# Kernel optimization log

Measured on AMD Instinct MI355X. Metric: run time of the kernel, lower is better.

The kernel has to match this reference:

```python
import jax, jax.numpy as jnp
import numpy as np

DIM = 512
WIN = 8
HEADS = 16
HEAD_DIM = DIM // HEADS
N = WIN * WIN
B_ = 1568


def _rel_pos_idx(window_size: int) -> np.ndarray:
    ch = np.arange(window_size)
    cw = np.arange(window_size)
    coords = np.stack(np.meshgrid(ch, cw, indexing='ij'))  # [2, W, W]
    flat = coords.reshape(2, -1)                            # [2, N]
    rel = flat[:, :, None] - flat[:, None, :]               # [2, N, N]
    rel = rel.transpose(1, 2, 0).copy()                     # [N, N, 2]
    rel[:, :, 0] += window_size - 1
    rel[:, :, 1] += window_size - 1
    rel[:, :, 0] *= 2 * window_size - 1
    return rel.sum(-1).astype(np.int32)                     # [N, N]


def setup_inputs() -> dict:
    key = jax.random.key(0)
    kx, kt, kq, kp, kb = jax.random.split(key, 5)
    x = jax.random.normal(kx, (B_, N, DIM), dtype=jnp.float32)
    # learned params
    table = jax.random.normal(kt, ((2 * WIN - 1) ** 2, HEADS), dtype=jnp.float32) * 0.02
    qkv_w = jax.random.normal(kq, (3 * DIM, DIM), dtype=jnp.float32) * (1.0 / np.sqrt(DIM))
    proj_w = jax.random.normal(kp, (DIM, DIM), dtype=jnp.float32) * (1.0 / np.sqrt(DIM))
    proj_b = jax.random.normal(kb, (DIM,), dtype=jnp.float32) * 0.02
    rel_idx = jnp.asarray(_rel_pos_idx(WIN))  # [N, N] int32
    return {"x": x, "qkv_w": qkv_w, "table": table, "proj_w": proj_w,
            "proj_b": proj_b, "rel_idx": rel_idx}


def reference(x, qkv_w, table, proj_w, proj_b, rel_idx):
    Bw, n, c = x.shape
    scale = jnp.sqrt(jnp.float32(HEAD_DIM))
    # qkv: Linear no-bias, torch weight [3C, C] -> x @ W^T
    qkv = (x @ qkv_w.T).reshape(Bw, n, 3, HEADS, HEAD_DIM)
    qkv = jnp.transpose(qkv, (2, 0, 3, 1, 4))  # [3, B, H, N, hd]
    q, k, v = qkv[0], qkv[1], qkv[2]
    attn = jnp.einsum('bhnd,bhmd->bhnm', q, k) / scale  # [B, H, N, N]
    bias = table[rel_idx]                                # [N, N, H]
    attn = attn + jnp.transpose(bias, (2, 0, 1))[None]   # [B, H, N, N]
    attn = jax.nn.softmax(attn, axis=-1)
    out = jnp.einsum('bhnm,bhmd->bhnd', attn, v)         # [B, H, N, hd]
    out = jnp.transpose(out, (0, 2, 1, 3)).reshape(Bw, n, c)
    return out @ proj_w.T + proj_b
```

## Files before the change

kernel.cpp:

```cpp
#include <hip/hip_runtime.h>
#include <stdint.h>

typedef unsigned short ushort_t;
typedef unsigned long long u64_t;
typedef __attribute__((ext_vector_type(4))) float f32x4;
typedef __attribute__((ext_vector_type(8))) short s16x8;

#define S1_ELEMS ((size_t)1568*64*512)

__device__ __forceinline__ ushort_t f2bf(float f) {
  unsigned u = __builtin_bit_cast(unsigned, f);
  u = u + 0x7fffu + ((u >> 16) & 1u);
  return (ushort_t)(u >> 16);
}

__device__ __forceinline__ void gl_lds16(const ushort_t* g, ushort_t* l) {
  typedef __attribute__((address_space(1))) void gvoid;
  typedef __attribute__((address_space(3))) void lvoid;
  __builtin_amdgcn_global_load_lds((gvoid*)(ushort_t*)g, (lvoid*)l, 16, 0, 0);
}

__global__ void k_prep(const float* __restrict__ x, ushort_t* __restrict__ xh,
                       const float* __restrict__ wq, ushort_t* __restrict__ wqh,
                       const float* __restrict__ wp, ushort_t* __restrict__ wph,
                       const float* __restrict__ table, const int* __restrict__ rel_idx,
                       float* __restrict__ bias) {
  int blk = blockIdx.x, tid = threadIdx.x;
  if (blk < 3136) {
    long i0 = (long)blk*256 + tid;
    #pragma unroll
    for (int rep = 0; rep < 8; rep++) {
      long i = i0 + (long)rep*802816;
      float4 v0 = ((const float4*)x)[2*i];
      float4 v1 = ((const float4*)x)[2*i + 1];
      s16x8 pk;
      pk[0] = (short)f2bf(v0.x); pk[1] = (short)f2bf(v0.y);
      pk[2] = (short)f2bf(v0.z); pk[3] = (short)f2bf(v0.w);
      pk[4] = (short)f2bf(v1.x); pk[5] = (short)f2bf(v1.y);
      pk[6] = (short)f2bf(v1.z); pk[7] = (short)f2bf(v1.w);
      *(s16x8*)&xh[i*8] = pk;
    }
  } else if (blk < 3648) {
    const float* src; ushort_t* dst; long i;
    if (blk < 3520) { src = wq; dst = wqh; i = (long)(blk - 3136)*256 + tid; }
    else            { src = wp; dst = wph; i = (long)(blk - 3520)*256 + tid; }
    float4 v0 = ((const float4*)src)[2*i];
    float4 v1 = ((const float4*)src)[2*i + 1];
    s16x8 pk;
    pk[0] = (short)f2bf(v0.x); pk[1] = (short)f2bf(v0.y);
    pk[2] = (short)f2bf(v0.z); pk[3] = (short)f2bf(v0.w);
    pk[4] = (short)f2bf(v1.x); pk[5] = (short)f2bf(v1.y);
    pk[6] = (short)f2bf(v1.z); pk[7] = (short)f2bf(v1.w);
    *(s16x8*)&dst[i*8] = pk;
  } else {
    int i0 = ((blk - 3648)*256 + tid)*4;
    #pragma unroll
    for (int j = 0; j < 4; j++) {
      int i = i0 + j;
      int h = i >> 12, rc = i & 4095;
      bias[i] = table[rel_idx[rc] * 16 + h];
    }
  }
}

struct GemmCtx {
  ushort_t* lds;
  const ushort_t *pA0, *pA1, *pB0, *pB1;
  int w, lane, wm, wn;
};

template<int BUFP, int KH, int RH, int SSEL, int SBUFP, int SU, int VM>
__device__ __forceinline__ void phase(const GemmCtx& C, f32x4 (&acc)[8][4], s16x8 (&bf)[4], int stau) {
  s16x8 af[4];
  #pragma unroll
  for (int t = 0; t < 4; t++)
    af[t] = *(const s16x8*)&C.lds[BUFP*32768 + ((C.wm*8 + RH*4 + t)*2 + KH)*512 + C.lane*8];
  if constexpr (RH == 0) {
    #pragma unroll
    for (int t = 0; t < 4; t++)
      bf[t] = *(const s16x8*)&C.lds[BUFP*32768 + 16384 + ((C.wn*4 + t)*2 + KH)*512 + C.lane*8];
  }
  if constexpr (SSEL == 0) {
    gl_lds16(C.pA0 + stau*64 + SU*32, C.lds + SBUFP*32768 + (4*C.w + SU)*512);
    gl_lds16(C.pA1 + stau*64 + SU*32, C.lds + SBUFP*32768 + (4*C.w + 2 + SU)*512);
  } else if constexpr (SSEL == 1) {
    gl_lds16(C.pB0 + stau*64 + SU*32, C.lds + SBUFP*32768 + 16384 + (4*C.w + SU)*512);
    gl_lds16(C.pB1 + stau*64 + SU*32, C.lds + SBUFP*32768 + 16384 + (4*C.w + 2 + SU)*512);
  }
  if constexpr (VM == 8) asm volatile("s_waitcnt vmcnt(8)" ::: "memory");
  else if constexpr (VM == 4) asm volatile("s_waitcnt vmcnt(4)" ::: "memory");
  else if constexpr (VM == 0) asm volatile("s_waitcnt vmcnt(0)" ::: "memory");
  __builtin_amdgcn_s_barrier();
  __builtin_amdgcn_s_setprio(1);
  #pragma unroll
  for (int ta = 0; ta < 4; ta++)
    #pragma unroll
    for (int tb = 0; tb < 4; tb++)
      acc[RH*4 + ta][tb] = __builtin_amdgcn_mfma_f32_16x16x32_bf16(af[ta], bf[tb], acc[RH*4 + ta][tb], 0, 0, 0);
  __builtin_amdgcn_s_setprio(0);
  __builtin_amdgcn_s_barrier();
}

template<int BUFP, bool S12, bool S34, int VM2, int VM4>
__device__ __forceinline__ void ktile(const GemmCtx& C, f32x4 (&acc)[8][4], int tau) {
  s16x8 bf[4];
  phase<BUFP, 0, 0, S12 ? 0 : -1, BUFP^1, 1, -1 >(C, acc, bf, tau + 1);
  phase<BUFP, 0, 1, S12 ? 1 : -1, BUFP^1, 1, VM2>(C, acc, bf, tau + 1);
  phase<BUFP, 1, 0, S34 ? 0 : -1, BUFP,   0, -1 >(C, acc, bf, tau + 2);
  phase<BUFP, 1, 1, S34 ? 1 : -1, BUFP,   0, VM4>(C, acc, bf, tau + 2);
}

__global__ __launch_bounds__(512, 2) void k_gemm_qkv(
    const ushort_t* __restrict__ xh, const ushort_t* __restrict__ wh,
    ushort_t* __restrict__ qh, ushort_t* __restrict__ kh, ushort_t* __restrict__ vt) {
  extern __shared__ __align__(16) ushort_t lds[];
  const int tid = threadIdx.x, w = tid >> 6, lane = tid & 63;
  const int g = lane >> 4, l15 = lane & 15;
  const int wm = w >> 2, wn = w & 3;
  int flat = blockIdx.x;
  int swz = (flat & 7) * 294 + (flat >> 3);
  int bx = swz % 6, by = swz / 6;

  GemmCtx C;
  C.lds = lds;
  C.pA0 = xh + ((size_t)by*256 + (size_t)(2*w)*16 + l15)*512 + g*8;
  C.pA1 = C.pA0 + 16*512;
  C.pB0 = wh + ((size_t)bx*256 + (size_t)(2*w)*16 + l15)*512 + g*8;
  C.pB1 = C.pB0 + 16*512;
  C.w = w; C.lane = lane; C.wm = wm; C.wn = wn;

  f32x4 acc[8][4];
  #pragma unroll
  for (int r = 0; r < 8; r++)
    #pragma unroll
    for (int c = 0; c < 4; c++) acc[r][c] = (f32x4){0.f, 0.f, 0.f, 0.f};

  gl_lds16(C.pA0 +  0, lds + (4*w + 0)*512);
  gl_lds16(C.pA1 +  0, lds + (4*w + 2)*512);
  gl_lds16(C.pB0 +  0, lds + 16384 + (4*w + 0)*512);
  gl_lds16(C.pB1 +  0, lds + 16384 + (4*w + 2)*512);
  gl_lds16(C.pA0 + 32, lds + (4*w + 1)*512);
  gl_lds16(C.pA1 + 32, lds + (4*w + 3)*512);
  gl_lds16(C.pB0 + 32, lds + 16384 + (4*w + 1)*512);
  gl_lds16(C.pB1 + 32, lds + 16384 + (4*w + 3)*512);
  gl_lds16(C.pA0 + 64, lds + 32768 + (4*w + 0)*512);
  gl_lds16(C.pA1 + 64, lds + 32768 + (4*w + 2)*512);
  gl_lds16(C.pB0 + 64, lds + 32768 + 16384 + (4*w + 0)*512);
  gl_lds16(C.pB1 + 64, lds + 32768 + 16384 + (4*w + 2)*512);
  asm volatile("s_waitcnt vmcnt(4)" ::: "memory");
  __builtin_amdgcn_s_barrier();

  for (int kt = 0; kt < 6; kt += 2) {
    ktile<0, true, true, 8, 8>(C, acc, kt);
    ktile<1, true, true, 8, 8>(C, acc, kt + 1);
  }
  ktile<0, true,  false, 8, 4>(C, acc, 6);
  ktile<1, false, false, 0, -1>(C, acc, 7);

  asm volatile("" ::: "memory");
  const int sel = bx >> 1;
  if (sel < 2) {
    #pragma unroll
    for (int ra = 0; ra < 8; ra++)
      #pragma unroll
      for (int tb = 0; tb < 4; tb++)
        #pragma unroll
        for (int j = 0; j < 4; j++) {
          int row = wm*128 + ra*16 + g*4 + j;
          int col = wn*64 + tb*16 + l15;
          int r = (row >> 6)*8 + (col >> 5);
          int n = row & 63, d = col & 31;
          int byte = r*4096 + ((n*64 + d*2) ^ ((n & 12) << 3));
          *(ushort_t*)((char*)lds + byte) = f2bf(acc[ra][tb][j]);
        }
  } else {
    #pragma unroll
    for (int ra = 0; ra < 8; ra++)
      #pragma unroll
      for (int tb = 0; tb < 4; tb++) {
        int row0 = wm*128 + ra*16 + g*4;
        int col = wn*64 + tb*16 + l15;
        int r = (row0 >> 6)*8 + (col >> 5);
        int n0 = row0 & 63, d = col & 31;
        u64_t pk = (u64_t)f2bf(acc[ra][tb][0])
                 | ((u64_t)f2bf(acc[ra][tb][1]) << 16)
                 | ((u64_t)f2bf(acc[ra][tb][2]) << 32)
                 | ((u64_t)f2bf(acc[ra][tb][3]) << 48);
        int byte = r*4096 + ((d*128 + n0*2) ^ ((d & 7) << 4) ^ (((((d >> 3) ^ (n0 >> 3))) & 1) << 6));
        *(u64_t*)((char*)lds + byte) = pk;
      }
  }
  asm volatile("s_waitcnt lgkmcnt(0)" ::: "memory");
  __builtin_amdgcn_s_barrier();
  ushort_t* dst = (sel == 0) ? qh : (sel == 1) ? kh : vt;
  const int hbase = (bx & 1) * 8;
  #pragma unroll
  for (int it = 0; it < 16; it++) {
    int cg = it*512 + tid;
    int r = cg >> 8, inner = cg & 255;
    int byte;
    if (sel < 2) byte = r*4096 + ((inner*16) ^ (((inner >> 2) & 12) << 3));
    else         byte = r*4096 + ((inner*16) ^ (((inner >> 3) & 7) << 4) ^ ((((inner >> 6) ^ inner) & 1) << 6));
    s16x8 v = *(const s16x8*)((const char*)lds + byte);
    int b = by*4 + (r >> 3), h = hbase + (r & 7);
    *(s16x8*)&dst[(size_t)(b*16 + h)*2048 + inner*8] = v;
  }
}

__device__ __forceinline__ void gemm256_loop(
    ushort_t* lds, const ushort_t* pA, const ushort_t* pB,
    int w, int lane, int wm, int wn, f32x4 (&acc)[8][4]) {
  #pragma unroll
  for (int q = 0; q < 2; q++) {
    gl_lds16(pA + q*8192 +  0, lds + ((2*w + q)*2 + 0)*512);
    gl_lds16(pA + q*8192 + 32, lds + ((2*w + q)*2 + 1)*512);
    gl_lds16(pB + q*8192 +  0, lds + 16384 + ((2*w + q)*2 + 0)*512);
    gl_lds16(pB + q*8192 + 32, lds + 16384 + ((2*w + q)*2 + 1)*512);
  }
  asm volatile("s_waitcnt vmcnt(0)" ::: "memory");
  __builtin_amdgcn_s_barrier();

  for (int tau = 0; tau < 8; ++tau) {
    ushort_t* bufR = lds + (tau & 1)*32768;
    ushort_t* bufW = lds + ((tau & 1) ^ 1)*32768;
    if (tau < 7) {
      int ko = (tau + 1)*64;
      #pragma unroll
      for (int q = 0; q < 2; q++) {
        gl_lds16(pA + q*8192 + ko,      bufW + ((2*w + q)*2 + 0)*512);
        gl_lds16(pA + q*8192 + ko + 32, bufW + ((2*w + q)*2 + 1)*512);
        gl_lds16(pB + q*8192 + ko,      bufW + 16384 + ((2*w + q)*2 + 0)*512);
        gl_lds16(pB + q*8192 + ko + 32, bufW + 16384 + ((2*w + q)*2 + 1)*512);
      }
    }
    s16x8 af[4][2], bf[4][2];
    #pragma unroll
    for (int t = 0; t < 4; t++)
      #pragma unroll
      for (int kh = 0; kh < 2; kh++) {
        af[t][kh] = *(const s16x8*)&bufR[((wm*8 + t)*2 + kh)*512 + lane*8];
        bf[t][kh] = *(const s16x8*)&bufR[16384 + ((wn*4 + t)*2 + kh)*512 + lane*8];
      }
    __builtin_amdgcn_s_barrier();
    asm volatile("s_waitcnt lgkmcnt(0)" ::: "memory");
    __builtin_amdgcn_sched_barrier(0);
    __builtin_amdgcn_s_setprio(1);
    #pragma unroll
    for (int t = 0; t < 4; t++)
      #pragma unroll
      for (int tb = 0; tb < 4; tb++) {
        acc[t][tb] = __builtin_amdgcn_mfma_f32_16x16x32_bf16(af[t][0], bf[tb][0], acc[t][tb], 0, 0, 0);
        acc[t][tb] = __builtin_amdgcn_mfma_f32_16x16x32_bf16(af[t][1], bf[tb][1], acc[t][tb], 0, 0, 0);
      }
    __builtin_amdgcn_s_setprio(0);
    s16x8 ag[4][2];
    #pragma unroll
    for (int t = 0; t < 4; t++)
      #pragma unroll
      for (int kh = 0; kh < 2; kh++)
        ag[t][kh] = *(const s16x8*)&bufR[((wm*8 + 4 + t)*2 + kh)*512 + lane*8];
    asm volatile("s_waitcnt lgkmcnt(0)" ::: "memory");
    __builtin_amdgcn_sched_barrier(0);
    __builtin_amdgcn_s_setprio(1);
    #pragma unroll
    for (int t = 0; t < 4; t++)
      #pragma unroll
      for (int tb = 0; tb < 4; tb++) {
        acc[4 + t][tb] = __builtin_amdgcn_mfma_f32_16x16x32_bf16(ag[t][0], bf[tb][0], acc[4 + t][tb], 0, 0, 0);
        acc[4 + t][tb] = __builtin_amdgcn_mfma_f32_16x16x32_bf16(ag[t][1], bf[tb][1], acc[4 + t][tb], 0, 0, 0);
      }
    __builtin_amdgcn_s_setprio(0);
    asm volatile("s_waitcnt vmcnt(0)" ::: "memory");
    __builtin_amdgcn_s_barrier();
  }
}

__global__ __launch_bounds__(512, 2) void k_gemm_proj(
    const ushort_t* __restrict__ ah, const ushort_t* __restrict__ wh,
    const float* __restrict__ pb, float* __restrict__ out) {
  extern __shared__ __align__(16) ushort_t lds[];
  const int tid = threadIdx.x, w = tid >> 6, lane = tid & 63;
  const int g = lane >> 4, l15 = lane & 15;
  const int wm = w >> 2, wn = w & 3;
  int flat = blockIdx.x;
  int swz = (flat & 7) * 98 + (flat >> 3);
  int bx = swz & 1, by = swz >> 1;

  const ushort_t* pA = ah + ((size_t)by*256 + (size_t)(2*w)*16 + l15)*512 + g*8;
  const ushort_t* pB = wh + ((size_t)bx*256 + (size_t)(2*w)*16 + l15)*512 + g*8;

  f32x4 acc[8][4];
  #pragma unroll
  for (int r = 0; r < 8; r++)
    #pragma unroll
    for (int c = 0; c < 4; c++) acc[r][c] = (f32x4){0.f, 0.f, 0.f, 0.f};

  gemm256_loop(lds, pA, pB, w, lane, wm, wn, acc);

  asm volatile("" ::: "memory");
  #pragma unroll
  for (int p = 0; p < 2; p++) {
    if (p) { asm volatile("" ::: "memory"); __builtin_amdgcn_s_barrier(); }
    if (wm == p) {
      #pragma unroll
      for (int ra = 0; ra < 8; ra++)
        #pragma unroll
        for (int tb = 0; tb < 4; tb++)
          #pragma unroll
          for (int j = 0; j < 4; j++) {
            int row = ra*16 + g*4 + j;
            int col = wn*64 + tb*16 + l15;
            int byte = (row*1024 + col*4) ^ ((row & 12) << 2) ^ ((row & 8) << 3);
            *(float*)((char*)lds + byte) = acc[ra][tb][j];
          }
    }
    asm volatile("s_waitcnt lgkmcnt(0)" ::: "memory");
    __builtin_amdgcn_s_barrier();
    #pragma unroll
    for (int it = 0; it < 16; it++) {
      int cg = it*512 + tid;
      int row = cg >> 6, c16 = cg & 63;
      int byte = row*1024 + ((c16*16) ^ ((row & 12) << 2) ^ ((row & 8) << 3));
      f32x4 v = *(const f32x4*)((const char*)lds + byte);
      int ncol = bx*256 + c16*4;
      f32x4 pbv = *(const f32x4*)&pb[ncol];
      v = v + pbv;
      *(f32x4*)&out[(size_t)(by*256 + p*128 + row)*512 + ncol] = v;
    }
  }
}

__global__ __launch_bounds__(256) void k_attn(
    const ushort_t* __restrict__ qh, const ushort_t* __restrict__ kh,
    const ushort_t* __restrict__ vt, const float* __restrict__ bias,
    ushort_t* __restrict__ aoh) {
  __shared__ ushort_t plds[4][4096];
  __shared__ float blds[64*68];
  const int tid = threadIdx.x, w = tid >> 6, lane = tid & 63;
  const int g = lane >> 4, l15 = lane & 15;
  const int h = blockIdx.x & 15;
  const int b = (blockIdx.x >> 4)*4 + w;
  const size_t base = (size_t)(b*16 + h) * 2048;

  s16x8 qf[4], kf[4];
  #pragma unroll
  for (int t = 0; t < 4; t++) {
    size_t o = base + (size_t)(t*16 + l15)*32 + g*8;
    qf[t] = *(const s16x8*)&qh[o];
    kf[t] = *(const s16x8*)&kh[o];
  }
  s16x8 vf[2][2];
  #pragma unroll
  for (int kt = 0; kt < 2; kt++)
    #pragma unroll
    for (int nt = 0; nt < 2; nt++)
      vf[kt][nt] = *(const s16x8*)&vt[base + (size_t)(nt*16 + l15)*64 + kt*32 + g*8];

  const float* bh_ = bias + ((size_t)h << 12);
  #pragma unroll
  for (int it = 0; it < 4; it++) {
    int idx = it*1024 + tid*4;
    int rr = idx >> 6, cc = idx & 63;
    *(f32x4*)&blds[rr*68 + cc] = *(const f32x4*)&bh_[idx];
  }
  __syncthreads();

  f32x4 s[4][4];
  #pragma unroll
  for (int r = 0; r < 4; r++)
    #pragma unroll
    for (int c = 0; c < 4; c++) s[r][c] = (f32x4){0.f,0.f,0.f,0.f};
  #pragma unroll
  for (int r = 0; r < 4; r++)
    #pragma unroll
    for (int c = 0; c < 4; c++)
      s[r][c] = __builtin_amdgcn_mfma_f32_16x16x32_bf16(qf[r], kf[c], s[r][c], 0, 0, 0);

  const float invs = 0.17677669529663687f;
  #pragma unroll
  for (int r = 0; r < 4; r++)
    #pragma unroll
    for (int c = 0; c < 4; c++)
      #pragma unroll
      for (int j = 0; j < 4; j++) {
        int rr = r*16 + g*4 + j, cc = c*16 + l15;
        s[r][c][j] = s[r][c][j]*invs + blds[rr*68 + cc];
      }

  #pragma unroll
  for (int r = 0; r < 4; r++)
    #pragma unroll
    for (int j = 0; j < 4; j++) {
      float mx = fmaxf(fmaxf(s[r][0][j], s[r][1][j]), fmaxf(s[r][2][j], s[r][3][j]));
      mx = fmaxf(mx, __shfl_xor(mx, 1));
      mx = fmaxf(mx, __shfl_xor(mx, 2));
      mx = fmaxf(mx, __shfl_xor(mx, 4));
      mx = fmaxf(mx, __shfl_xor(mx, 8));
      float p0 = __expf(s[r][0][j]-mx), p1 = __expf(s[r][1][j]-mx);
      float p2 = __expf(s[r][2][j]-mx), p3 = __expf(s[r][3][j]-mx);
      float sum = p0 + p1 + p2 + p3;
      sum += __shfl_xor(sum, 1);
      sum += __shfl_xor(sum, 2);
      sum += __shfl_xor(sum, 4);
      sum += __shfl_xor(sum, 8);
      float rv = 1.0f / sum;
      s[r][0][j] = p0*rv; s[r][1][j] = p1*rv; s[r][2][j] = p2*rv; s[r][3][j] = p3*rv;
    }

  ushort_t* Pw = plds[w];
  asm volatile("s_waitcnt lgkmcnt(0)" ::: "memory");
  __builtin_amdgcn_sched_barrier(0);
  #pragma unroll
  for (int r = 0; r < 4; r++)
    #pragma unroll
    for (int c = 0; c < 4; c++)
      #pragma unroll
      for (int j = 0; j < 4; j++) {
        int idx = ((c >> 1)*4 + r)*512 + ((((c & 1)*2) + (l15 >> 3))*16 + g*4 + j)*8 + (l15 & 7);
        Pw[idx] = f2bf(s[r][c][j]);
      }
  asm volatile("s_waitcnt lgkmcnt(0)" ::: "memory");
  __builtin_amdgcn_sched_barrier(0);

  s16x8 pf[4][2];
  #pragma unroll
  for (int ta = 0; ta < 4; ta++)
    #pragma unroll
    for (int kt = 0; kt < 2; kt++)
      pf[ta][kt] = *(const s16x8*)&Pw[(kt*4 + ta)*512 + lane*8];

  f32x4 o[4][2];
  #pragma unroll
  for (int ta = 0; ta < 4; ta++)
    #pragma unroll
    for (int nt = 0; nt < 2; nt++) o[ta][nt] = (f32x4){0.f,0.f,0.f,0.f};
  #pragma unroll
  for (int ta = 0; ta < 4; ta++)
    #pragma unroll
    for (int nt = 0; nt < 2; nt++)
      #pragma unroll
      for (int kt = 0; kt < 2; kt++)
        o[ta][nt] = __builtin_amdgcn_mfma_f32_16x16x32_bf16(pf[ta][kt], vf[kt][nt], o[ta][nt], 0, 0, 0);

  #pragma unroll
  for (int ta = 0; ta < 4; ta++)
    #pragma unroll
    for (int nt = 0; nt < 2; nt++)
      #pragma unroll
      for (int j = 0; j < 4; j++) {
        int rr = ta*16 + g*4 + j, dd = nt*16 + l15;
        aoh[((size_t)b*64 + rr)*512 + h*32 + dd] = f2bf(o[ta][nt][j]);
      }
}

extern "C" void kernel_launch(void* const* d_in, const int* in_sizes, int n_in,
                              void* d_out, int out_size, void* d_ws, size_t ws_size,
                              hipStream_t stream) {
  const float* x      = (const float*)d_in[0];
  const float* qkv_w  = (const float*)d_in[1];
  const float* table  = (const float*)d_in[2];
  const float* proj_w = (const float*)d_in[3];
  const float* proj_b = (const float*)d_in[4];
  const int*   rel_idx = (const int*)d_in[5];

  const size_t S1 = S1_ELEMS;
  const size_t need = (4*S1 + 786432 + 262144)*sizeof(ushort_t) + 65536*sizeof(float);
  if (ws_size < need) return;

  ushort_t* qh  = (ushort_t*)d_ws;
  ushort_t* kh  = qh + S1;
  ushort_t* vt  = kh + S1;
  ushort_t* xh  = vt + S1;
  ushort_t* wqh = xh + S1;
  ushort_t* wph = wqh + 786432;
  float*    bias = (float*)(wph + 262144);
  ushort_t* aoh = xh;

  hipFuncSetAttribute((const void*)k_gemm_qkv,
                      hipFuncAttributeMaxDynamicSharedMemorySize, 131072);
  hipFuncSetAttribute((const void*)k_gemm_proj,
                      hipFuncAttributeMaxDynamicSharedMemorySize, 131072);

  k_prep<<<3712, 256, 0, stream>>>(x, xh, qkv_w, wqh, proj_w, wph, table, rel_idx, bias);
  k_gemm_qkv<<<2352, 512, 131072, stream>>>(xh, wqh, qh, kh, vt);
  k_attn<<<6272, 256, 0, stream>>>(qh, kh, vt, bias, aoh);
  k_gemm_proj<<<784, 512, 131072, stream>>>(aoh, wph, proj_b, (float*)d_out);
}
```

Before: 505.2 us.

## Shrink QKV GEMM tile to 128x256 with triple-buffered K pipeline

```diff
diff --git a/kernel.cpp b/kernel.cpp
--- a/kernel.cpp
+++ b/kernel.cpp
@@ -63,54 +63,7 @@
   }
 }
 
-struct GemmCtx {
-  ushort_t* lds;
-  const ushort_t *pA0, *pA1, *pB0, *pB1;
-  int w, lane, wm, wn;
-};
-
-template<int BUFP, int KH, int RH, int SSEL, int SBUFP, int SU, int VM>
-__device__ __forceinline__ void phase(const GemmCtx& C, f32x4 (&acc)[8][4], s16x8 (&bf)[4], int stau) {
-  s16x8 af[4];
-  #pragma unroll
-  for (int t = 0; t < 4; t++)
-    af[t] = *(const s16x8*)&C.lds[BUFP*32768 + ((C.wm*8 + RH*4 + t)*2 + KH)*512 + C.lane*8];
-  if constexpr (RH == 0) {
-    #pragma unroll
-    for (int t = 0; t < 4; t++)
-      bf[t] = *(const s16x8*)&C.lds[BUFP*32768 + 16384 + ((C.wn*4 + t)*2 + KH)*512 + C.lane*8];
-  }
-  if constexpr (SSEL == 0) {
-    gl_lds16(C.pA0 + stau*64 + SU*32, C.lds + SBUFP*32768 + (4*C.w + SU)*512);
-    gl_lds16(C.pA1 + stau*64 + SU*32, C.lds + SBUFP*32768 + (4*C.w + 2 + SU)*512);
-  } else if constexpr (SSEL == 1) {
-    gl_lds16(C.pB0 + stau*64 + SU*32, C.lds + SBUFP*32768 + 16384 + (4*C.w + SU)*512);
-    gl_lds16(C.pB1 + stau*64 + SU*32, C.lds + SBUFP*32768 + 16384 + (4*C.w + 2 + SU)*512);
-  }
-  if constexpr (VM == 8) asm volatile("s_waitcnt vmcnt(8)" ::: "memory");
-  else if constexpr (VM == 4) asm volatile("s_waitcnt vmcnt(4)" ::: "memory");
-  else if constexpr (VM == 0) asm volatile("s_waitcnt vmcnt(0)" ::: "memory");
-  __builtin_amdgcn_s_barrier();
-  __builtin_amdgcn_s_setprio(1);
-  #pragma unroll
-  for (int ta = 0; ta < 4; ta++)
-    #pragma unroll
-    for (int tb = 0; tb < 4; tb++)
-      acc[RH*4 + ta][tb] = __builtin_amdgcn_mfma_f32_16x16x32_bf16(af[ta], bf[tb], acc[RH*4 + ta][tb], 0, 0, 0);
-  __builtin_amdgcn_s_setprio(0);
-  __builtin_amdgcn_s_barrier();
-}
-
-template<int BUFP, bool S12, bool S34, int VM2, int VM4>
-__device__ __forceinline__ void ktile(const GemmCtx& C, f32x4 (&acc)[8][4], int tau) {
-  s16x8 bf[4];
-  phase<BUFP, 0, 0, S12 ? 0 : -1, BUFP^1, 1, -1 >(C, acc, bf, tau + 1);
-  phase<BUFP, 0, 1, S12 ? 1 : -1, BUFP^1, 1, VM2>(C, acc, bf, tau + 1);
-  phase<BUFP, 1, 0, S34 ? 0 : -1, BUFP,   0, -1 >(C, acc, bf, tau + 2);
-  phase<BUFP, 1, 1, S34 ? 1 : -1, BUFP,   0, VM4>(C, acc, bf, tau + 2);
-}
-
-__global__ __launch_bounds__(512, 2) void k_gemm_qkv(
+__global__ __launch_bounds__(512, 4) void k_gemm_qkv(
     const ushort_t* __restrict__ xh, const ushort_t* __restrict__ wh,
     ushort_t* __restrict__ qh, ushort_t* __restrict__ kh, ushort_t* __restrict__ vt) {
   extern __shared__ __align__(16) ushort_t lds[];
@@ -118,92 +71,106 @@
   const int g = lane >> 4, l15 = lane & 15;
   const int wm = w >> 2, wn = w & 3;
   int flat = blockIdx.x;
-  int swz = (flat & 7) * 294 + (flat >> 3);
+  int swz = (flat & 7) * 588 + (flat >> 3);
   int bx = swz % 6, by = swz / 6;
 
-  GemmCtx C;
-  C.lds = lds;
-  C.pA0 = xh + ((size_t)by*256 + (size_t)(2*w)*16 + l15)*512 + g*8;
-  C.pA1 = C.pA0 + 16*512;
-  C.pB0 = wh + ((size_t)bx*256 + (size_t)(2*w)*16 + l15)*512 + g*8;
-  C.pB1 = C.pB0 + 16*512;
-  C.w = w; C.lane = lane; C.wm = wm; C.wn = wn;
-
-  f32x4 acc[8][4];
-  #pragma unroll
-  for (int r = 0; r < 8; r++)
+  const ushort_t* pA  = xh + ((size_t)(by*128 + w*16 + l15))*512 + g*8;
+  const ushort_t* pB0 = wh + ((size_t)(bx*256 + (2*w)*16 + l15))*512 + g*8;
+  const ushort_t* pB1 = pB0 + 16*512;
+
+  f32x4 acc[4][4];
+  #pragma unroll
+  for (int r = 0; r < 4; r++)
     #pragma unroll
     for (int c = 0; c < 4; c++) acc[r][c] = (f32x4){0.f, 0.f, 0.f, 0.f};
 
-  gl_lds16(C.pA0 +  0, lds + (4*w + 0)*512);
-  gl_lds16(C.pA1 +  0, lds + (4*w + 2)*512);
-  gl_lds16(C.pB0 +  0, lds + 16384 + (4*w + 0)*512);
-  gl_lds16(C.pB1 +  0, lds + 16384 + (4*w + 2)*512);
-  gl_lds16(C.pA0 + 32, lds + (4*w + 1)*512);
-  gl_lds16(C.pA1 + 32, lds + (4*w + 3)*512);
-  gl_lds16(C.pB0 + 32, lds + 16384 + (4*w + 1)*512);
-  gl_lds16(C.pB1 + 32, lds + 16384 + (4*w + 3)*512);
-  gl_lds16(C.pA0 + 64, lds + 32768 + (4*w + 0)*512);
-  gl_lds16(C.pA1 + 64, lds + 32768 + (4*w + 2)*512);
-  gl_lds16(C.pB0 + 64, lds + 32768 + 16384 + (4*w + 0)*512);
-  gl_lds16(C.pB1 + 64, lds + 32768 + 16384 + (4*w + 2)*512);
-  asm volatile("s_waitcnt vmcnt(4)" ::: "memory");
+  #pragma unroll
+  for (int t0 = 0; t0 < 2; t0++) {
+    ushort_t* buf = lds + t0*12288;
+    gl_lds16(pA  + t0*32, buf + w*512);
+    gl_lds16(pB0 + t0*32, buf + 4096 + (2*w)*512);
+    gl_lds16(pB1 + t0*32, buf + 4096 + (2*w + 1)*512);
+  }
+
+  #pragma unroll
+  for (int t = 0; t < 16; ++t) {
+    if (t == 15) asm volatile("s_waitcnt vmcnt(0)" ::: "memory");
+    else         asm volatile("s_waitcnt vmcnt(3)" ::: "memory");
+    __builtin_amdgcn_s_barrier();
+    if (t < 14) {
+      ushort_t* bufS = lds + ((t + 2) % 3)*12288;
+      gl_lds16(pA  + (t + 2)*32, bufS + w*512);
+      gl_lds16(pB0 + (t + 2)*32, bufS + 4096 + (2*w)*512);
+      gl_lds16(pB1 + (t + 2)*32, bufS + 4096 + (2*w + 1)*512);
+    }
+    ushort_t* buf = lds + (t % 3)*12288;
+    s16x8 af[4], bf[4];
+    #pragma unroll
+    for (int ta = 0; ta < 4; ta++)
+      af[ta] = *(const s16x8*)&buf[(wm*4 + ta)*512 + lane*8];
+    #pragma unroll
+    for (int tb = 0; tb < 4; tb++)
+      bf[tb] = *(const s16x8*)&buf[4096 + (wn*4 + tb)*512 + lane*8];
+    __builtin_amdgcn_s_setprio(1);
+    #pragma unroll
+    for (int ta = 0; ta < 4; ta++)
+      #pragma unroll
+      for (int tb = 0; tb < 4; tb++)
+        acc[ta][tb] = __builtin_amdgcn_mfma_f32_16x16x32_bf16(af[ta], bf[tb], acc[ta][tb], 0, 0, 0);
+    __builtin_amdgcn_s_setprio(0);
+  }
+
   __builtin_amdgcn_s_barrier();
-
-  for (int kt = 0; kt < 6; kt += 2) {
-    ktile<0, true, true, 8, 8>(C, acc, kt);
-    ktile<1, true, true, 8, 8>(C, acc, kt + 1);
-  }
-  ktile<0, true,  false, 8, 4>(C, acc, 6);
-  ktile<1, false, false, 0, -1>(C, acc, 7);
-
-  asm volatile("" ::: "memory");
   const int sel = bx >> 1;
-  if (sel < 2) {
-    #pragma unroll
-    for (int ra = 0; ra < 8; ra++)
-      #pragma unroll
-      for (int tb = 0; tb < 4; tb++)
-        #pragma unroll
-        for (int j = 0; j < 4; j++) {
-          int row = wm*128 + ra*16 + g*4 + j;
-          int col = wn*64 + tb*16 + l15;
-          int r = (row >> 6)*8 + (col >> 5);
-          int n = row & 63, d = col & 31;
-          int byte = r*4096 + ((n*64 + d*2) ^ ((n & 12) << 3));
-          *(ushort_t*)((char*)lds + byte) = f2bf(acc[ra][tb][j]);
-        }
-  } else {
-    #pragma unroll
-    for (int ra = 0; ra < 8; ra++)
-      #pragma unroll
-      for (int tb = 0; tb < 4; tb++) {
-        int row0 = wm*128 + ra*16 + g*4;
-        int col = wn*64 + tb*16 + l15;
-        int r = (row0 >> 6)*8 + (col >> 5);
-        int n0 = row0 & 63, d = col & 31;
-        u64_t pk = (u64_t)f2bf(acc[ra][tb][0])
-                 | ((u64_t)f2bf(acc[ra][tb][1]) << 16)
-                 | ((u64_t)f2bf(acc[ra][tb][2]) << 32)
-                 | ((u64_t)f2bf(acc[ra][tb][3]) << 48);
-        int byte = r*4096 + ((d*128 + n0*2) ^ ((d & 7) << 4) ^ (((((d >> 3) ^ (n0 >> 3))) & 1) << 6));
-        *(u64_t*)((char*)lds + byte) = pk;
-      }
-  }
-  asm volatile("s_waitcnt lgkmcnt(0)" ::: "memory");
-  __builtin_amdgcn_s_barrier();
   ushort_t* dst = (sel == 0) ? qh : (sel == 1) ? kh : vt;
   const int hbase = (bx & 1) * 8;
   #pragma unroll
-  for (int it = 0; it < 16; it++) {
-    int cg = it*512 + tid;
-    int r = cg >> 8, inner = cg & 255;
-    int byte;
-    if (sel < 2) byte = r*4096 + ((inner*16) ^ (((inner >> 2) & 12) << 3));
-    else         byte = r*4096 + ((inner*16) ^ (((inner >> 3) & 7) << 4) ^ ((((inner >> 6) ^ inner) & 1) << 6));
-    s16x8 v = *(const s16x8*)((const char*)lds + byte);
-    int b = by*4 + (r >> 3), h = hbase + (r & 7);
-    *(s16x8*)&dst[(size_t)(b*16 + h)*2048 + inner*8] = v;
+  for (int p = 0; p < 2; p++) {
+    if (p) { asm volatile("" ::: "memory"); __builtin_amdgcn_s_barrier(); }
+    if (wm == p) {
+      if (sel < 2) {
+        #pragma unroll
+        for (int ta = 0; ta < 4; ta++)
+          #pragma unroll
+          for (int tb = 0; tb < 4; tb++)
+            #pragma unroll
+            for (int j = 0; j < 4; j++) {
+              int n = ta*16 + g*4 + j;
+              int lc = wn*64 + tb*16 + l15;
+              int r = lc >> 5, d = lc & 31;
+              int byte = r*4096 + ((n*64 + d*2) ^ ((n & 12) << 3));
+              *(ushort_t*)((char*)lds + byte) = f2bf(acc[ta][tb][j]);
+            }
+      } else {
+        #pragma unroll
+        for (int ta = 0; ta < 4; ta++)
+          #pragma unroll
+          for (int tb = 0; tb < 4; tb++) {
+            int n0 = ta*16 + g*4;
+            int lc = wn*64 + tb*16 + l15;
+            int r = lc >> 5, d = lc & 31;
+            u64_t pk = (u64_t)f2bf(acc[ta][tb][0])
+                     | ((u64_t)f2bf(acc[ta][tb][1]) << 16)
+                     | ((u64_t)f2bf(acc[ta][tb][2]) << 32)
+                     | ((u64_t)f2bf(acc[ta][tb][3]) << 48);
+            int byte = r*4096 + ((d*128 + n0*2) ^ ((d & 7) << 4) ^ (((((d >> 3) ^ (n0 >> 3))) & 1) << 6));
+            *(u64_t*)((char*)lds + byte) = pk;
+          }
+      }
+    }
+    asm volatile("s_waitcnt lgkmcnt(0)" ::: "memory");
+    __builtin_amdgcn_s_barrier();
+    #pragma unroll
+    for (int it = 0; it < 4; it++) {
+      int cg = it*512 + tid;
+      int r = cg >> 8, inner = cg & 255;
+      int byte;
+      if (sel < 2) byte = r*4096 + ((inner*16) ^ (((inner >> 2) & 12) << 3));
+      else         byte = r*4096 + ((inner*16) ^ (((inner >> 3) & 7) << 4) ^ ((((inner >> 6) ^ inner) & 1) << 6));
+      s16x8 v = *(const s16x8*)((const char*)lds + byte);
+      int b = by*2 + p, h = hbase + r;
+      *(s16x8*)&dst[(size_t)(b*16 + h)*2048 + inner*8] = v;
+    }
   }
 }
 
@@ -477,12 +444,12 @@
   ushort_t* aoh = xh;
 
   hipFuncSetAttribute((const void*)k_gemm_qkv,
-                      hipFuncAttributeMaxDynamicSharedMemorySize, 131072);
+                      hipFuncAttributeMaxDynamicSharedMemorySize, 73728);
   hipFuncSetAttribute((const void*)k_gemm_proj,
                       hipFuncAttributeMaxDynamicSharedMemorySize, 131072);
 
   k_prep<<<3712, 256, 0, stream>>>(x, xh, qkv_w, wqh, proj_w, wph, table, rel_idx, bias);
-  k_gemm_qkv<<<2352, 512, 131072, stream>>>(xh, wqh, qh, kh, vt);
+  k_gemm_qkv<<<4704, 512, 73728, stream>>>(xh, wqh, qh, kh, vt);
   k_attn<<<6272, 256, 0, stream>>>(qh, kh, vt, bias, aoh);
   k_gemm_proj<<<784, 512, 131072, stream>>>(aoh, wph, proj_b, (float*)d_out);
 }
```

New measurement: 531.4 us. 1.05x slower.
